# Kernel optimization log

Measured on AMD Instinct MI355X. Metric: run time of the kernel, lower is better.

The kernel has to match this reference:

```python
import jax, jax.numpy as jnp
import numpy as np

B, S, A, M = 131072, 376, 17, 5
H1, H2 = 400, 300
LOG_STD_MIN, LOG_STD_MAX = -10.0, 2.0
EPIS_MIN, EPIS_MAX = 4.53999297624848e-05, 7.38905609893065


def _uniform(k, shape, fan_in):
    bound = 1.0 / np.sqrt(fan_in)
    return jax.random.uniform(k, shape, jnp.float32, -bound, bound)


def setup_inputs() -> dict:
    key = jax.random.key(0)
    ks = jax.random.split(key, 8)
    W1 = _uniform(ks[0], (S, H1), S); b1 = _uniform(ks[1], (H1,), S)
    W2 = _uniform(ks[2], (H1, H2), H1); b2 = _uniform(ks[3], (H2,), H1)
    W3 = _uniform(ks[4], (H2, A * M * 3), H2); b3 = _uniform(ks[5], (A * M * 3,), H2)
    state = jax.random.normal(ks[6], (B, S), jnp.float32)
    eps = jax.random.normal(ks[7], (B, A), jnp.float32)
    return {"state": state, "eps": eps, "W1": W1, "b1": b1, "W2": W2, "b2": b2, "W3": W3, "b3": b3}


def _mixture_stats(state, W1, b1, W2, b2, W3, b3):
    h = jax.nn.relu(state @ W1 + b1)
    h = jax.nn.relu(h @ W2 + b2)
    out = jnp.tanh(h @ W3 + b3)                      # [B, 3*A*M]
    mw, mm, lms = jnp.split(out, 3, axis=-1)
    mw = mw.reshape(-1, A, M)
    mm = mm.reshape(-1, A, M)
    lms = lms.reshape(-1, A, M)
    w = jax.nn.softmax(mw, axis=2)                   # max-subtraction is built in
    std = jnp.exp(jnp.clip(lms, LOG_STD_MIN, LOG_STD_MAX))
    mean = jnp.sum(w * mm, axis=2)                   # [B, A]
    alea = jnp.sum(w * std, axis=2)
    epis = jnp.sum(w * jnp.square(mm - mean[:, :, None]), axis=2)
    epis = jnp.clip(epis, EPIS_MIN, EPIS_MAX)
    return mean, alea + epis, epis


def _diag_logprob(x, mean, std):
    # MVN with covariance diag(std^2) == independent diagonal Gaussian
    z = (x - mean) / std
    d = x.shape[-1]
    return -0.5 * jnp.sum(z * z + 2.0 * jnp.log(std), axis=-1) - 0.5 * d * jnp.log(2.0 * jnp.pi).astype(x.dtype)


def reference(state, eps, W1, b1, W2, b2, W3, b3):
    mean, total, epis = _mixture_stats(state, W1, b1, W2, b2, W3, b3)
    sample = mean + total * eps                      # rsample of N(mean, diag(total^2))
    tanh_sample = jnp.tanh(sample)
    lp_ttl = _diag_logprob(sample, mean, total)
    lp_eps = _diag_logprob(sample, mean, epis)
    corr = jnp.sum(jnp.log(1.0 - jnp.square(tanh_sample) + 1e-6), axis=1, keepdims=True)
    log_pi_ttl = lp_ttl[:, None] - corr
    log_pi_eps = lp_eps[:, None] - corr
    return tanh_sample, log_pi_ttl, log_pi_eps
```

## Files before the change

### kernel.cpp

```cpp
#include <hip/hip_runtime.h>

typedef _Float16 half8 __attribute__((ext_vector_type(8)));
typedef float floatx4 __attribute__((ext_vector_type(4)));

#define BATCH 131072
#define S_DIM 376
#define NACT 17

#define L1_NT 28
#define L1_CH 12
#define L2_NT 20
#define L2_CH 13
#define L3_NT 16
#define L3_CH 10
#define L1F 0
#define L2F (L1_NT * L1_CH * 1024)
#define L3F (L2F + L2_NT * L2_CH * 1024)
#define WTOTF (L3F + L3_NT * L3_CH * 1024)

#define ROWS 32
#define AW1 416
#define AW2 328
#define OW3 260
#define LDS_BYTES 53248

#define MFMA16(a, b, c) __builtin_amdgcn_mfma_f32_16x16x32_f16(a, b, c, 0, 0, 0)

__global__ __launch_bounds__(256) void prep_kernel(const float* __restrict__ W1,
                                                   const float* __restrict__ W2,
                                                   const float* __restrict__ W3,
                                                   _Float16* __restrict__ ws) {
  int idx = blockIdx.x * 256 + threadIdx.x;
  if (idx >= WTOTF) return;
  const float* W;
  int CH, NR, KR, e = idx;
  if (e < L2F) {
    W = W1; CH = L1_CH; NR = 400; KR = 376;
  } else if (e < L3F) {
    W = W2; CH = L2_CH; NR = 300; KR = 400; e -= L2F;
  } else {
    W = W3; CH = L3_CH; NR = 255; KR = 300; e -= L3F;
  }
  const int f = e >> 10, r = e & 1023;
  const int plane = r >> 9, rr = r & 511;
  const int lane = rr >> 3, j = rr & 7;
  const int q = lane >> 4, m = lane & 15;
  const int ntile = f / CH, kc = f - ntile * CH;
  const int n = ntile * 16 + m, k = kc * 32 + q * 8 + j;
  const float v = (n < NR && k < KR) ? W[k * NR + n] : 0.f;
  const _Float16 hi = (_Float16)v;
  ws[idx] = plane ? (_Float16)(v - (float)hi) : hi;
}

template <int AW, bool SWZ>
__device__ __forceinline__ half8 lds_frag(const char* base, int row, int koff) {
  int off = (row * AW + koff) * 2;
  if (SWZ) off ^= (row & 7) << 4;
  return *(const half8*)(base + off);
}

template <int NT, int CHUNKS, int AW, bool SWZ, int I>
struct KStep {
  static constexpr int TOT = NT * CHUNKS;
  static __device__ __forceinline__ void run(const char* Ahi, const char* Alo,
                                             const _Float16* bb, int m, int kq,
                                             half8 (&bh)[5], half8 (&bl)[5],
                                             half8 (&ah)[2], half8 (&al)[2],
                                             half8 (&ahn)[2], half8 (&aln)[2],
                                             floatx4 (&acc)[2][NT]) {
    constexpr int nt = I % NT;
    constexpr int kc = I / NT;
    constexpr int s = I % 5;
    if constexpr (I + 4 < TOT) {
      constexpr int j = I + 4;
      constexpr int fo = ((j % NT) * CHUNKS + (j / NT)) * 1024;
      bh[j % 5] = *(const half8*)(bb + fo);
      bl[j % 5] = *(const half8*)(bb + fo + 512);
    }
    if constexpr (nt == NT - 2 && kc + 1 < CHUNKS) {
      ahn[0] = lds_frag<AW, SWZ>(Ahi, m, (kc + 1) * 32 + kq);
      ahn[1] = lds_frag<AW, SWZ>(Ahi, 16 + m, (kc + 1) * 32 + kq);
      aln[0] = lds_frag<AW, SWZ>(Alo, m, (kc + 1) * 32 + kq);
      aln[1] = lds_frag<AW, SWZ>(Alo, 16 + m, (kc + 1) * 32 + kq);
    }
    __builtin_amdgcn_sched_barrier(0);
    acc[0][nt] = MFMA16(ah[0], bh[s], acc[0][nt]);
    acc[1][nt] = MFMA16(ah[1], bh[s], acc[1][nt]);
    acc[0][nt] = MFMA16(ah[0], bl[s], acc[0][nt]);
    acc[1][nt] = MFMA16(ah[1], bl[s], acc[1][nt]);
    acc[0][nt] = MFMA16(al[0], bh[s], acc[0][nt]);
    acc[1][nt] = MFMA16(al[1], bh[s], acc[1][nt]);
    if constexpr (nt == NT - 1 && kc + 1 < CHUNKS) {
      ah[0] = ahn[0]; ah[1] = ahn[1]; al[0] = aln[0]; al[1] = aln[1];
    }
    if constexpr (I + 1 < TOT)
      KStep<NT, CHUNKS, AW, SWZ, I + 1>::run(Ahi, Alo, bb, m, kq, bh, bl, ah, al, ahn, aln, acc);
  }
};

template <int NT, int CHUNKS, int AW, bool SWZ>
__device__ __forceinline__ void gemm_layer(const _Float16* __restrict__ Ahi_,
                                           const _Float16* __restrict__ Alo_,
                                           const _Float16* __restrict__ Bf,
                                           int ntile0, int lane, int q, int m,
                                           floatx4 (&acc)[2][NT]) {
  const char* Ahi = (const char*)Ahi_;
  const char* Alo = (const char*)Alo_;
  const int kq = q * 8;
  const _Float16* bb = Bf + ntile0 * CHUNKS * 1024 + lane * 8;

  half8 bh[5], bl[5];
  half8 ah[2], al[2], ahn[2], aln[2];

  ah[0] = lds_frag<AW, SWZ>(Ahi, m, kq);
  ah[1] = lds_frag<AW, SWZ>(Ahi, 16 + m, kq);
  al[0] = lds_frag<AW, SWZ>(Alo, m, kq);
  al[1] = lds_frag<AW, SWZ>(Alo, 16 + m, kq);
  bh[0] = *(const half8*)(bb + 0 * CHUNKS * 1024);
  bl[0] = *(const half8*)(bb + 0 * CHUNKS * 1024 + 512);
  bh[1] = *(const half8*)(bb + 1 * CHUNKS * 1024);
  bl[1] = *(const half8*)(bb + 1 * CHUNKS * 1024 + 512);
  bh[2] = *(const half8*)(bb + 2 * CHUNKS * 1024);
  bl[2] = *(const half8*)(bb + 2 * CHUNKS * 1024 + 512);
  bh[3] = *(const half8*)(bb + 3 * CHUNKS * 1024);
  bl[3] = *(const half8*)(bb + 3 * CHUNKS * 1024 + 512);
  __builtin_amdgcn_sched_barrier(0);

  KStep<NT, CHUNKS, AW, SWZ, 0>::run(Ahi, Alo, bb, m, kq, bh, bl, ah, al, ahn, aln, acc);
}

__global__ __launch_bounds__(256, 3) void actor_kernel(const float* __restrict__ state,
                                                       const float* __restrict__ eps,
                                                       const float* __restrict__ b1,
                                                       const float* __restrict__ b2,
                                                       const float* __restrict__ b3,
                                                       const _Float16* __restrict__ wsp,
                                                       float* __restrict__ out) {
  extern __shared__ char smem[];
  _Float16* Ahi = (_Float16*)smem;
  _Float16* Alo = Ahi + ROWS * AW1;

  const int t = threadIdx.x;
  const int wave = t >> 6;
  const int lane = t & 63;
  const int q = lane >> 4;
  const int m = lane & 15;
  const long rowbase = (long)blockIdx.x * ROWS;

  {
    const int row = t >> 3, p = t & 7;
    const long gbase = (rowbase + row) * S_DIM;
#pragma unroll
    for (int c0 = 0; c0 < 6; ++c0) {
      const int col = c0 * 64 + p * 8;
      float v[8];
      if (col + 8 <= S_DIM) {
        const float4* sp = (const float4*)(state + gbase + col);
        float4 x0 = sp[0], x1 = sp[1];
        v[0] = x0.x; v[1] = x0.y; v[2] = x0.z; v[3] = x0.w;
        v[4] = x1.x; v[5] = x1.y; v[6] = x1.z; v[7] = x1.w;
      } else {
#pragma unroll
        for (int j = 0; j < 8; ++j) v[j] = 0.f;
      }
      half8 h, l;
#pragma unroll
      for (int j = 0; j < 8; ++j) {
        _Float16 hi = (_Float16)v[j];
        h[j] = hi;
        l[j] = (_Float16)(v[j] - (float)hi);
      }
      int off = (row * AW1 + col) * 2;
      off ^= (row & 7) << 4;
      *(half8*)((char*)Ahi + off) = h;
      *(half8*)((char*)Alo + off) = l;
    }
  }
  __syncthreads();

  floatx4 acc1[2][7];
#pragma unroll
  for (int a = 0; a < 2; ++a)
#pragma unroll
    for (int b = 0; b < 7; ++b) { acc1[a][b][0] = 0.f; acc1[a][b][1] = 0.f; acc1[a][b][2] = 0.f; acc1[a][b][3] = 0.f; }
  gemm_layer<7, 12, AW1, true>(Ahi, Alo, wsp + L1F, wave * 7, lane, q, m, acc1);

  __syncthreads();
  _Float16* H1hi = Ahi;
  _Float16* H1lo = Alo;
#pragma unroll
  for (int nt = 0; nt < 7; ++nt) {
    const int tile = wave * 7 + nt;
    if (tile < 26) {
      const int col = tile * 16 + m;
      const float bias = (col < 400) ? b1[col] : 0.f;
#pragma unroll
      for (int mt = 0; mt < 2; ++mt)
#pragma unroll
        for (int r = 0; r < 4; ++r) {
          const int row = mt * 16 + q * 4 + r;
          float v = fmaxf(acc1[mt][nt][r] + bias, 0.f);
          _Float16 hi = (_Float16)v;
          int off = (row * AW1 + col) * 2;
          off ^= (row & 7) << 4;
          *(_Float16*)((char*)H1hi + off) = hi;
          *(_Float16*)((char*)H1lo + off) = (_Float16)(v - (float)hi);
        }
    }
  }
  __syncthreads();

  floatx4 acc2[2][5];
#pragma unroll
  for (int a = 0; a < 2; ++a)
#pragma unroll
    for (int b = 0; b < 5; ++b) { acc2[a][b][0] = 0.f; acc2[a][b][1] = 0.f; acc2[a][b][2] = 0.f; acc2[a][b][3] = 0.f; }
  gemm_layer<5, 13, AW1, true>(H1hi, H1lo, wsp + L2F, wave * 5, lane, q, m, acc2);

  __syncthreads();
  _Float16* H2hi = (_Float16*)smem;
  _Float16* H2lo = H2hi + ROWS * AW2;
#pragma unroll
  for (int nt = 0; nt < 5; ++nt) {
    const int col = (wave * 5 + nt) * 16 + m;
    const float bias = (col < 300) ? b2[col] : 0.f;
#pragma unroll
    for (int mt = 0; mt < 2; ++mt)
#pragma unroll
      for (int r = 0; r < 4; ++r) {
        const int row = mt * 16 + q * 4 + r;
        float v = fmaxf(acc2[mt][nt][r] + bias, 0.f);
        _Float16 hi = (_Float16)v;
        H2hi[row * AW2 + col] = hi;
        H2lo[row * AW2 + col] = (_Float16)(v - (float)hi);
      }
  }
  __syncthreads();

  floatx4 acc3[2][4];
#pragma unroll
  for (int a = 0; a < 2; ++a)
#pragma unroll
    for (int b = 0; b < 4; ++b) { acc3[a][b][0] = 0.f; acc3[a][b][1] = 0.f; acc3[a][b][2] = 0.f; acc3[a][b][3] = 0.f; }
  gemm_layer<4, 10, AW2, false>(H2hi, H2lo, wsp + L3F, wave * 4, lane, q, m, acc3);

  __syncthreads();
  float* O3 = (float*)smem;
#pragma unroll
  for (int nt = 0; nt < 4; ++nt) {
    const int col = (wave * 4 + nt) * 16 + m;
    const float bias = (col < 255) ? b3[col] : 0.f;
#pragma unroll
    for (int mt = 0; mt < 2; ++mt)
#pragma unroll
      for (int r = 0; r < 4; ++r) {
        const int row = mt * 16 + q * 4 + r;
        O3[row * OW3 + col] = tanhf(acc3[mt][nt][r] + bias);
      }
  }
  __syncthreads();

  {
    const int row = t >> 3, p = t & 7;
    const long gr = rowbase + row;
    const float* Or = O3 + row * OW3;
    float pc = 0.f, pt = 0.f, pe = 0.f;
    const int nact = (p == 0) ? 3 : 2;
    for (int ia = 0; ia < nact; ++ia) {
      const int a = p + ia * 8;
      float mw[5], mmv[5], lms[5];
#pragma unroll
      for (int j = 0; j < 5; ++j) {
        mw[j]  = Or[a * 5 + j];
        mmv[j] = Or[85 + a * 5 + j];
        lms[j] = Or[170 + a * 5 + j];
      }
      float w[5], es = 0.f;
#pragma unroll
      for (int j = 0; j < 5; ++j) { w[j] = expf(mw[j]); es += w[j]; }
      const float inv = 1.f / es;
      float mean = 0.f;
#pragma unroll
      for (int j = 0; j < 5; ++j) { w[j] *= inv; mean += w[j] * mmv[j]; }
      float alea = 0.f, epis = 0.f;
#pragma unroll
      for (int j = 0; j < 5; ++j) {
        float sd = expf(fminf(fmaxf(lms[j], -10.f), 2.f));
        alea += w[j] * sd;
        float d = mmv[j] - mean;
        epis += w[j] * d * d;
      }
      epis = fminf(fmaxf(epis, 4.53999297624848e-05f), 7.38905609893065f);
      const float total = alea + epis;
      const float ea = eps[gr * NACT + a];
      const float sample = mean + total * ea;
      const float ts = tanhf(sample);
      out[gr * NACT + a] = ts;
      pc += logf(1.f - ts * ts + 1e-6f);
      const float dz = sample - mean;
      const float zt = dz / total;
      const float ze = dz / epis;
      pt += zt * zt + 2.f * logf(total);
      pe += ze * ze + 2.f * logf(epis);
    }
    pc += __shfl_xor(pc, 1); pc += __shfl_xor(pc, 2); pc += __shfl_xor(pc, 4);
    pt += __shfl_xor(pt, 1); pt += __shfl_xor(pt, 2); pt += __shfl_xor(pt, 4);
    pe += __shfl_xor(pe, 1); pe += __shfl_xor(pe, 2); pe += __shfl_xor(pe, 4);
    if (p == 0) {
      const float hdl2pi = 15.62195506447944f;
      out[(long)NACT * BATCH + gr] = (-0.5f * pt - hdl2pi) - pc;
      out[(long)(NACT + 1) * BATCH + gr] = (-0.5f * pe - hdl2pi) - pc;
    }
  }
}

extern "C" void kernel_launch(void* const* d_in, const int* in_sizes, int n_in,
                              void* d_out, int out_size, void* d_ws, size_t ws_size,
                              hipStream_t stream) {
  const float* state = (const float*)d_in[0];
  const float* eps   = (const float*)d_in[1];
  const float* W1    = (const float*)d_in[2];
  const float* b1    = (const float*)d_in[3];
  const float* W2    = (const float*)d_in[4];
  const float* b2    = (const float*)d_in[5];
  const float* W3    = (const float*)d_in[6];
  const float* b3    = (const float*)d_in[7];
  float* out = (float*)d_out;
  _Float16* ws = (_Float16*)d_ws;

  (void)in_sizes; (void)n_in; (void)out_size; (void)ws_size;

  prep_kernel<<<(WTOTF + 255) / 256, 256, 0, stream>>>(W1, W2, W3, ws);
  actor_kernel<<<BATCH / ROWS, 256, LDS_BYTES, stream>>>(state, eps, b1, b2, b3, ws, out);
}
```

Before: 543.8 us.

## Stream weight fragments through per-wave LDS ring via direct global-to-LDS loads

Replaces the register-resident 5-deep prefetch of weight fragments with a 3-slot per-wave LDS ring filled by global_load_lds DMA, with explicit vmcnt waits. This cuts the VGPRs held for B fragments, so the min-blocks-per-SM launch bound is dropped. LDS per block grows by 24 KB, which may lower occupancy, and it adds LDS reads plus waitcnt stalls in the inner MFMA loop.

New measurement: 612.9 us. 1.13x slower.

```diff
diff --git a/kernel.cpp b/kernel.cpp
--- a/kernel.cpp
+++ b/kernel.cpp
@@ -22,7 +22,8 @@
 #define AW1 416
 #define AW2 328
 #define OW3 260
-#define LDS_BYTES 53248
+#define BRING_OFF 53248
+#define LDS_BYTES (53248 + 4 * 3 * 2048)
 
 #define MFMA16(a, b, c) __builtin_amdgcn_mfma_f32_16x16x32_f16(a, b, c, 0, 0, 0)
 
@@ -52,6 +53,15 @@
   ws[idx] = plane ? (_Float16)(v - (float)hi) : hi;
 }
 
+__device__ __forceinline__ void dma16(const _Float16* g, char* l) {
+  __builtin_amdgcn_global_load_lds(
+      (const __attribute__((address_space(1))) void*)g,
+      (__attribute__((address_space(3))) void*)l, 16, 0, 0);
+}
+__device__ __forceinline__ void wait_vm0() { asm volatile("s_waitcnt vmcnt(0)" ::: "memory"); }
+__device__ __forceinline__ void wait_vm2() { asm volatile("s_waitcnt vmcnt(2)" ::: "memory"); }
+__device__ __forceinline__ void wait_vm4() { asm volatile("s_waitcnt vmcnt(4)" ::: "memory"); }
+
 template <int AW, bool SWZ>
 __device__ __forceinline__ half8 lds_frag(const char* base, int row, int koff) {
   int off = (row * AW + koff) * 2;
@@ -63,19 +73,20 @@
 struct KStep {
   static constexpr int TOT = NT * CHUNKS;
   static __device__ __forceinline__ void run(const char* Ahi, const char* Alo,
-                                             const _Float16* bb, int m, int kq,
-                                             half8 (&bh)[5], half8 (&bl)[5],
+                                             const _Float16* bbg, char* bring,
+                                             int lane16, int m, int kq,
+                                             half8 (&bh)[2], half8 (&bl)[2],
                                              half8 (&ah)[2], half8 (&al)[2],
                                              half8 (&ahn)[2], half8 (&aln)[2],
                                              floatx4 (&acc)[2][NT]) {
     constexpr int nt = I % NT;
     constexpr int kc = I / NT;
-    constexpr int s = I % 5;
-    if constexpr (I + 4 < TOT) {
-      constexpr int j = I + 4;
-      constexpr int fo = ((j % NT) * CHUNKS + (j / NT)) * 1024;
-      bh[j % 5] = *(const half8*)(bb + fo);
-      bl[j % 5] = *(const half8*)(bb + fo + 512);
+    constexpr int cs = I & 1, ns = cs ^ 1;
+    if constexpr (I + 1 < TOT) {
+      if constexpr (I + 2 < TOT) wait_vm2(); else wait_vm0();
+      const char* slot = (const char*)bring + ((I + 1) % 3) * 2048;
+      bh[ns] = *(const half8*)(slot + lane16);
+      bl[ns] = *(const half8*)(slot + 1024 + lane16);
     }
     if constexpr (nt == NT - 2 && kc + 1 < CHUNKS) {
       ahn[0] = lds_frag<AW, SWZ>(Ahi, m, (kc + 1) * 32 + kq);
@@ -84,17 +95,25 @@
       aln[1] = lds_frag<AW, SWZ>(Alo, 16 + m, (kc + 1) * 32 + kq);
     }
     __builtin_amdgcn_sched_barrier(0);
-    acc[0][nt] = MFMA16(ah[0], bh[s], acc[0][nt]);
-    acc[1][nt] = MFMA16(ah[1], bh[s], acc[1][nt]);
-    acc[0][nt] = MFMA16(ah[0], bl[s], acc[0][nt]);
-    acc[1][nt] = MFMA16(ah[1], bl[s], acc[1][nt]);
-    acc[0][nt] = MFMA16(al[0], bh[s], acc[0][nt]);
-    acc[1][nt] = MFMA16(al[1], bh[s], acc[1][nt]);
+    acc[0][nt] = MFMA16(ah[0], bh[cs], acc[0][nt]);
+    acc[1][nt] = MFMA16(ah[1], bh[cs], acc[1][nt]);
+    acc[0][nt] = MFMA16(ah[0], bl[cs], acc[0][nt]);
+    acc[1][nt] = MFMA16(ah[1], bl[cs], acc[1][nt]);
+    acc[0][nt] = MFMA16(al[0], bh[cs], acc[0][nt]);
+    acc[1][nt] = MFMA16(al[1], bh[cs], acc[1][nt]);
     if constexpr (nt == NT - 1 && kc + 1 < CHUNKS) {
       ah[0] = ahn[0]; ah[1] = ahn[1]; al[0] = aln[0]; al[1] = aln[1];
     }
+    if constexpr (I + 3 < TOT) {
+      __builtin_amdgcn_sched_barrier(0);
+      constexpr int fo = (((I + 3) % NT) * CHUNKS + ((I + 3) / NT)) * 1024;
+      char* dslot = bring + (I % 3) * 2048;
+      dma16(bbg + fo, dslot);
+      dma16(bbg + fo + 512, dslot + 1024);
+    }
     if constexpr (I + 1 < TOT)
-      KStep<NT, CHUNKS, AW, SWZ, I + 1>::run(Ahi, Alo, bb, m, kq, bh, bl, ah, al, ahn, aln, acc);
+      KStep<NT, CHUNKS, AW, SWZ, I + 1>::run(Ahi, Alo, bbg, bring, lane16, m, kq,
+                                             bh, bl, ah, al, ahn, aln, acc);
   }
 };
 
@@ -102,40 +121,42 @@
 __device__ __forceinline__ void gemm_layer(const _Float16* __restrict__ Ahi_,
                                            const _Float16* __restrict__ Alo_,
                                            const _Float16* __restrict__ Bf,
+                                           char* bring,
                                            int ntile0, int lane, int q, int m,
                                            floatx4 (&acc)[2][NT]) {
   const char* Ahi = (const char*)Ahi_;
   const char* Alo = (const char*)Alo_;
   const int kq = q * 8;
-  const _Float16* bb = Bf + ntile0 * CHUNKS * 1024 + lane * 8;
-
-  half8 bh[5], bl[5];
+  const int lane16 = lane * 16;
+  const _Float16* bbg = Bf + ntile0 * CHUNKS * 1024 + lane * 8;
+
+  half8 bh[2], bl[2];
   half8 ah[2], al[2], ahn[2], aln[2];
 
+#pragma unroll
+  for (int s = 0; s < 3; ++s) {
+    dma16(bbg + s * CHUNKS * 1024, bring + s * 2048);
+    dma16(bbg + s * CHUNKS * 1024 + 512, bring + s * 2048 + 1024);
+  }
   ah[0] = lds_frag<AW, SWZ>(Ahi, m, kq);
   ah[1] = lds_frag<AW, SWZ>(Ahi, 16 + m, kq);
   al[0] = lds_frag<AW, SWZ>(Alo, m, kq);
   al[1] = lds_frag<AW, SWZ>(Alo, 16 + m, kq);
-  bh[0] = *(const half8*)(bb + 0 * CHUNKS * 1024);
-  bl[0] = *(const half8*)(bb + 0 * CHUNKS * 1024 + 512);
-  bh[1] = *(const half8*)(bb + 1 * CHUNKS * 1024);
-  bl[1] = *(const half8*)(bb + 1 * CHUNKS * 1024 + 512);
-  bh[2] = *(const half8*)(bb + 2 * CHUNKS * 1024);
-  bl[2] = *(const half8*)(bb + 2 * CHUNKS * 1024 + 512);
-  bh[3] = *(const half8*)(bb + 3 * CHUNKS * 1024);
-  bl[3] = *(const half8*)(bb + 3 * CHUNKS * 1024 + 512);
-  __builtin_amdgcn_sched_barrier(0);
-
-  KStep<NT, CHUNKS, AW, SWZ, 0>::run(Ahi, Alo, bb, m, kq, bh, bl, ah, al, ahn, aln, acc);
-}
-
-__global__ __launch_bounds__(256, 3) void actor_kernel(const float* __restrict__ state,
-                                                       const float* __restrict__ eps,
-                                                       const float* __restrict__ b1,
-                                                       const float* __restrict__ b2,
-                                                       const float* __restrict__ b3,
-                                                       const _Float16* __restrict__ wsp,
-                                                       float* __restrict__ out) {
+  wait_vm4();
+  bh[0] = *(const half8*)((const char*)bring + lane16);
+  bl[0] = *(const half8*)((const char*)bring + 1024 + lane16);
+
+  KStep<NT, CHUNKS, AW, SWZ, 0>::run(Ahi, Alo, bbg, bring, lane16, m, kq,
+                                     bh, bl, ah, al, ahn, aln, acc);
+}
+
+__global__ __launch_bounds__(256) void actor_kernel(const float* __restrict__ state,
+                                                    const float* __restrict__ eps,
+                                                    const float* __restrict__ b1,
+                                                    const float* __restrict__ b2,
+                                                    const float* __restrict__ b3,
+                                                    const _Float16* __restrict__ wsp,
+                                                    float* __restrict__ out) {
   extern __shared__ char smem[];
   _Float16* Ahi = (_Float16*)smem;
   _Float16* Alo = Ahi + ROWS * AW1;
@@ -145,6 +166,7 @@
   const int lane = t & 63;
   const int q = lane >> 4;
   const int m = lane & 15;
+  char* bring = smem + BRING_OFF + wave * (3 * 2048);
   const long rowbase = (long)blockIdx.x * ROWS;
 
   {
@@ -183,7 +205,7 @@
   for (int a = 0; a < 2; ++a)
 #pragma unroll
     for (int b = 0; b < 7; ++b) { acc1[a][b][0] = 0.f; acc1[a][b][1] = 0.f; acc1[a][b][2] = 0.f; acc1[a][b][3] = 0.f; }
-  gemm_layer<7, 12, AW1, true>(Ahi, Alo, wsp + L1F, wave * 7, lane, q, m, acc1);
+  gemm_layer<7, 12, AW1, true>(Ahi, Alo, wsp + L1F, bring, wave * 7, lane, q, m, acc1);
 
   __syncthreads();
   _Float16* H1hi = Ahi;
@@ -215,7 +237,7 @@
   for (int a = 0; a < 2; ++a)
 #pragma unroll
     for (int b = 0; b < 5; ++b) { acc2[a][b][0] = 0.f; acc2[a][b][1] = 0.f; acc2[a][b][2] = 0.f; acc2[a][b][3] = 0.f; }
-  gemm_layer<5, 13, AW1, true>(H1hi, H1lo, wsp + L2F, wave * 5, lane, q, m, acc2);
+  gemm_layer<5, 13, AW1, true>(H1hi, H1lo, wsp + L2F, bring, wave * 5, lane, q, m, acc2);
 
   __syncthreads();
   _Float16* H2hi = (_Float16*)smem;
@@ -242,7 +264,7 @@
   for (int a = 0; a < 2; ++a)
 #pragma unroll
     for (int b = 0; b < 4; ++b) { acc3[a][b][0] = 0.f; acc3[a][b][1] = 0.f; acc3[a][b][2] = 0.f; acc3[a][b][3] = 0.f; }
-  gemm_layer<4, 10, AW2, false>(H2hi, H2lo, wsp + L3F, wave * 4, lane, q, m, acc3);
+  gemm_layer<4, 10, AW2, false>(H2hi, H2lo, wsp + L3F, bring, wave * 4, lane, q, m, acc3);
 
   __syncthreads();
   float* O3 = (float*)smem;
@@ -330,6 +352,9 @@
 
   (void)in_sizes; (void)n_in; (void)out_size; (void)ws_size;
 
+  hipFuncSetAttribute(reinterpret_cast<const void*>(actor_kernel),
+                      hipFuncAttributeMaxDynamicSharedMemorySize, LDS_BYTES);
+
   prep_kernel<<<(WTOTF + 255) / 256, 256, 0, stream>>>(W1, W2, W3, ws);
   actor_kernel<<<BATCH / ROWS, 256, LDS_BYTES, stream>>>(state, eps, b1, b2, b3, ws, out);
 }
```
